# Performance work log

Hardware: AMD Instinct MI355X
Metric: run time of the kernel (lower is better)

Reference implementation:

```python
import jax, jax.numpy as jnp
import numpy as np

B, L, NC = 65536, 1024, 4
C_PHYS = 4000.0       # wave speed in PhysicsConsistencyLoss
WIN = 20              # window_size
SAMPLE_RATE = 20000
C_WE, DX, DT = 1.0, 0.1, 0.01  # WaveEquationLoss defaults
W_WAVE, W_PHYS = 0.1, 0.1


def setup_inputs() -> dict:
    key = jax.random.key(0)
    k1, k2, k3, k4 = jax.random.split(key, 4)
    waveform = jax.random.normal(k1, (B, L), dtype=jnp.float32)
    logits = jax.random.normal(k2, (B, NC), dtype=jnp.float32)
    # depths in [0, 100) -> t_positions = depth*10 in [0, 1000), inside the 1024-sample trace
    defect_depth = jax.random.uniform(k3, (B, 1), dtype=jnp.float32) * 100.0
    labels = jax.random.randint(k4, (B,), 0, NC, dtype=jnp.int64)
    return {"waveform": waveform, "logits": logits,
            "defect_depth": defect_depth, "labels": labels}


def _second_diff(w):
    # interior: w[i+1] - 2 w[i] + w[i-1]; boundaries replicate the torch code exactly
    inner = w[:, 2:] - 2.0 * w[:, 1:-1] + w[:, :-2]
    b0 = (w[:, 1] - w[:, 0])[:, None]          # w1 - 2w0 + w0
    bL = (w[:, -2] - w[:, -1])[:, None]        # w[-1] - 2w[-1] + w[-2]
    return jnp.concatenate([b0, inner, bL], axis=1)


def _wave_eq_loss(w):
    d2 = _second_diff(w)
    d2u_dt2 = d2 / (DT ** 2)
    d2u_dx2 = d2 / (DX ** 2)
    residual = d2u_dt2 - (C_WE ** 2) * d2u_dx2
    return jnp.mean(residual ** 2)


def _physics_consistency_loss(waveform, pred_depth, pred_class):
    bsz, length = waveform.shape
    t_positions = (2.0 * pred_depth[:, 0] / C_PHYS) * SAMPLE_RATE   # (B,)
    t = jnp.linspace(0.0, length - 1, length, dtype=waveform.dtype)  # (L,)
    sigma = WIN / 4.0
    win = jnp.exp(-0.5 * ((t[None, :] - t_positions[:, None]) / sigma) ** 2)  # (B, L)
    win = win / jnp.sum(win, axis=1, keepdims=True)
    energies = jnp.sum(waveform ** 2 * win, axis=1)          # (B,)
    energies = energies / (WIN * jnp.max(waveform))
    is_defect = (pred_class == 2) | (pred_class == 3)
    pen_defect = jnp.where(energies < 0.1, (0.1 - energies) ** 2, 0.0)
    pen_clean = jnp.where(energies > 0.5, (energies - 0.5) ** 2, 0.0)
    penalty = jnp.where(is_defect, pen_defect, pen_clean)
    return jnp.sum(penalty) / bsz


def reference(waveform, logits, defect_depth, labels):
    # masked cross-entropy (labels == -1 ignored)
    mask = labels != -1
    safe_labels = jnp.where(mask, labels, 0)
    logp = jax.nn.log_softmax(logits, axis=-1)
    nll = -jnp.take_along_axis(logp, safe_labels[:, None], axis=1)[:, 0]
    n_valid = jnp.sum(mask)
    cls_loss = jnp.where(n_valid > 0,
                         jnp.sum(jnp.where(mask, nll, 0.0)) / jnp.maximum(n_valid, 1),
                         0.0)
    wave_loss = _wave_eq_loss(waveform)
    pred_class = jnp.argmax(logits, axis=1)
    physics_loss = _physics_consistency_loss(waveform, defect_depth, pred_class)
    total = cls_loss + W_WAVE * wave_loss + W_PHYS * physics_loss
    return (total, cls_loss, wave_loss, physics_loss)
```

## Files before the change

### kernel.cpp

```cpp
#include <hip/hip_runtime.h>
#include <math.h>

#define NROWS 65536
#define LLEN  1024
#define RBLOCKS (NROWS / 8)
#define CBLOCKS (NROWS / 256)

struct Acc {
    double d2_sum;
    float  gmax;
};

__device__ __forceinline__ void row_compute(const float4* f, int lane, float tpos,
                                            float& d2s, float& mx,
                                            float& wsum, float& wesum) {
    d2s = 0.0f; mx = -INFINITY; wsum = 0.0f; wesum = 0.0f;
#pragma unroll
    for (int p = 0; p < 4; ++p) {
        const float x0 = f[p].x, x1 = f[p].y, x2 = f[p].z, x3 = f[p].w;

        float left  = __shfl_up(x3, 1, 64);
        float right = __shfl_down(x0, 1, 64);
        const float prevTail = __shfl((p > 0) ? f[p - 1].w : x0, 63, 64);
        const float nextHead = __shfl((p < 3) ? f[p + 1].x : x3, 0, 64);
        if (lane == 0)  left  = (p > 0) ? prevTail : x0;
        if (lane == 63) right = (p < 3) ? nextHead : x2;

        const float d2a = x1 - 2.0f * x0 + left;
        const float d2b = x2 - 2.0f * x1 + x0;
        const float d2c = x3 - 2.0f * x2 + x1;
        const float d2d = right - 2.0f * x3 + x2;
        d2s += d2a * d2a + d2b * d2b + d2c * d2c + d2d * d2d;

        mx = fmaxf(fmaxf(mx, fmaxf(x0, x1)), fmaxf(x2, x3));

        const float pstart = (float)(p * 256);
        if (tpos > pstart - 75.0f && tpos < pstart + 330.0f) {
            const float e0 = pstart + (float)(4 * lane);
#pragma unroll
            for (int j = 0; j < 4; ++j) {
                const float c = (j == 0) ? x0 : (j == 1) ? x1 : (j == 2) ? x2 : x3;
                const float dt = (e0 + (float)j - tpos) * 0.2f;
                const float g = __expf(-0.5f * dt * dt);
                wsum  += g;
                wesum += c * c * g;
            }
        }
    }
}

__global__ __launch_bounds__(256) void row_kernel(const float* __restrict__ wf,
                                                  const float* __restrict__ depth,
                                                  float* __restrict__ eraw,
                                                  float* __restrict__ d2_part,
                                                  float* __restrict__ mx_part) {
    __shared__ float s_d2[4], s_mx[4];
    const int wave = threadIdx.x >> 6;
    const int lane = threadIdx.x & 63;
    const int r0 = (blockIdx.x * 4 + wave) * 2;

    const float4* srcA = (const float4*)(wf + (size_t)r0 * LLEN);
    const float4* srcB = srcA + (LLEN / 4);
    float4 fA[4], fB[4];
#pragma unroll
    for (int p = 0; p < 4; ++p) fA[p] = srcA[p * 64 + lane];
#pragma unroll
    for (int p = 0; p < 4; ++p) fB[p] = srcB[p * 64 + lane];
    const float2 dep = *(const float2*)(depth + r0);

    float d2sA, mxA, wsA, weA, d2sB, mxB, wsB, weB;
    row_compute(fA, lane, dep.x * 10.0f, d2sA, mxA, wsA, weA);
    row_compute(fB, lane, dep.y * 10.0f, d2sB, mxB, wsB, weB);

#pragma unroll
    for (int off = 32; off > 0; off >>= 1) {
        wsA += __shfl_down(wsA, off, 64);
        weA += __shfl_down(weA, off, 64);
        wsB += __shfl_down(wsB, off, 64);
        weB += __shfl_down(weB, off, 64);
    }
    float d2s = d2sA + d2sB;
    float mx  = fmaxf(mxA, mxB);
#pragma unroll
    for (int off = 32; off > 0; off >>= 1) {
        d2s += __shfl_down(d2s, off, 64);
        mx = fmaxf(mx, __shfl_down(mx, off, 64));
    }

    if (lane == 0) {
        eraw[r0]     = weA / wsA;
        eraw[r0 + 1] = weB / wsB;
        s_d2[wave] = d2s;
        s_mx[wave] = mx;
    }
    __syncthreads();
    if (threadIdx.x == 0) {
        d2_part[blockIdx.x] = s_d2[0] + s_d2[1] + s_d2[2] + s_d2[3];
        mx_part[blockIdx.x] = fmaxf(fmaxf(s_mx[0], s_mx[1]), fmaxf(s_mx[2], s_mx[3]));
    }
}

__global__ __launch_bounds__(256) void reduce_kernel(const float* __restrict__ d2_part,
                                                     const float* __restrict__ mx_part,
                                                     Acc* __restrict__ acc) {
    __shared__ double s_d2[4];
    __shared__ float  s_mx[4];
    const int wave = threadIdx.x >> 6;
    const int lane = threadIdx.x & 63;

    double d2 = 0.0;
    float mx = -INFINITY;
    for (int i = threadIdx.x; i < RBLOCKS; i += 256) {
        d2 += (double)d2_part[i];
        mx = fmaxf(mx, mx_part[i]);
    }
#pragma unroll
    for (int off = 32; off > 0; off >>= 1) {
        d2 += __shfl_down(d2, off, 64);
        mx = fmaxf(mx, __shfl_down(mx, off, 64));
    }
    if (lane == 0) { s_d2[wave] = d2; s_mx[wave] = mx; }
    __syncthreads();
    if (threadIdx.x == 0) {
        acc->d2_sum = s_d2[0] + s_d2[1] + s_d2[2] + s_d2[3];
        acc->gmax   = fmaxf(fmaxf(s_mx[0], s_mx[1]), fmaxf(s_mx[2], s_mx[3]));
    }
}

__global__ __launch_bounds__(256) void cls_kernel(const float* __restrict__ logits,
                                                  const int* __restrict__ labels,
                                                  const float* __restrict__ eraw,
                                                  const Acc* __restrict__ acc,
                                                  float* __restrict__ nll_part,
                                                  float* __restrict__ pen_part,
                                                  int* __restrict__ nv_part) {
    __shared__ float s_nll[4], s_pen[4];
    __shared__ int   s_nv[4];
    const int wave = threadIdx.x >> 6;
    const int lane = threadIdx.x & 63;
    const int r = blockIdx.x * 256 + threadIdx.x;

    const float4 lg = ((const float4*)logits)[r];
    const float m = fmaxf(fmaxf(lg.x, lg.y), fmaxf(lg.z, lg.w));
    const float lse = m + logf(__expf(lg.x - m) + __expf(lg.y - m) +
                               __expf(lg.z - m) + __expf(lg.w - m));

    const int lab = labels[r];
    const bool valid = (lab != -1);
    const int sl = valid ? lab : 0;
    const float lv = (sl == 0) ? lg.x : (sl == 1) ? lg.y : (sl == 2) ? lg.z : lg.w;
    float nll = valid ? (lse - lv) : 0.0f;

    int pc = 0; float bv = lg.x;
    if (lg.y > bv) { bv = lg.y; pc = 1; }
    if (lg.z > bv) { bv = lg.z; pc = 2; }
    if (lg.w > bv) { bv = lg.w; pc = 3; }

    const float E = eraw[r] / (20.0f * acc->gmax);
    const bool isdef = (pc == 2) || (pc == 3);
    float pen;
    if (isdef) pen = (E < 0.1f) ? (0.1f - E) * (0.1f - E) : 0.0f;
    else       pen = (E > 0.5f) ? (E - 0.5f) * (E - 0.5f) : 0.0f;

    const unsigned long long bal = __ballot(valid);
#pragma unroll
    for (int off = 32; off > 0; off >>= 1) {
        nll += __shfl_down(nll, off, 64);
        pen += __shfl_down(pen, off, 64);
    }
    if (lane == 0) { s_nll[wave] = nll; s_pen[wave] = pen; s_nv[wave] = __popcll(bal); }
    __syncthreads();
    if (threadIdx.x == 0) {
        nll_part[blockIdx.x] = s_nll[0] + s_nll[1] + s_nll[2] + s_nll[3];
        pen_part[blockIdx.x] = s_pen[0] + s_pen[1] + s_pen[2] + s_pen[3];
        nv_part[blockIdx.x]  = s_nv[0] + s_nv[1] + s_nv[2] + s_nv[3];
    }
}

__global__ __launch_bounds__(256) void final_kernel(const float* __restrict__ nll_part,
                                                    const float* __restrict__ pen_part,
                                                    const int* __restrict__ nv_part,
                                                    const Acc* __restrict__ acc,
                                                    float* __restrict__ out) {
    __shared__ double s_nll[4], s_pen[4];
    __shared__ int    s_nv[4];
    const int wave = threadIdx.x >> 6;
    const int lane = threadIdx.x & 63;

    double nll = (double)nll_part[threadIdx.x];
    double pen = (double)pen_part[threadIdx.x];
    int nv = nv_part[threadIdx.x];
#pragma unroll
    for (int off = 32; off > 0; off >>= 1) {
        nll += __shfl_down(nll, off, 64);
        pen += __shfl_down(pen, off, 64);
        nv  += __shfl_down(nv,  off, 64);
    }
    if (lane == 0) { s_nll[wave] = nll; s_pen[wave] = pen; s_nv[wave] = nv; }
    __syncthreads();
    if (threadIdx.x == 0) {
        const double nll_s = s_nll[0] + s_nll[1] + s_nll[2] + s_nll[3];
        const double pen_s = s_pen[0] + s_pen[1] + s_pen[2] + s_pen[3];
        const int    nv_s  = s_nv[0] + s_nv[1] + s_nv[2] + s_nv[3];
        const double cls  = (nv_s > 0) ? nll_s / (double)nv_s : 0.0;
        const double wave_l = acc->d2_sum * (9900.0 * 9900.0) / ((double)NROWS * (double)LLEN);
        const double phys = pen_s / (double)NROWS;
        out[0] = (float)(cls + 0.1 * wave_l + 0.1 * phys);
        out[1] = (float)cls;
        out[2] = (float)wave_l;
        out[3] = (float)phys;
    }
}

extern "C" void kernel_launch(void* const* d_in, const int* in_sizes, int n_in,
                              void* d_out, int out_size, void* d_ws, size_t ws_size,
                              hipStream_t stream) {
    const float* wf     = (const float*)d_in[0];
    const float* logits = (const float*)d_in[1];
    const float* depth  = (const float*)d_in[2];
    const int*   labels = (const int*)d_in[3];
    float* out = (float*)d_out;

    char* ws = (char*)d_ws;
    Acc*   acc      = (Acc*)ws;                       ws += 256;
    float* eraw     = (float*)ws;                     ws += NROWS * sizeof(float);
    float* d2_part  = (float*)ws;                     ws += RBLOCKS * sizeof(float);
    float* mx_part  = (float*)ws;                     ws += RBLOCKS * sizeof(float);
    float* nll_part = (float*)ws;                     ws += CBLOCKS * sizeof(float);
    float* pen_part = (float*)ws;                     ws += CBLOCKS * sizeof(float);
    int*   nv_part  = (int*)ws;

    row_kernel<<<RBLOCKS, 256, 0, stream>>>(wf, depth, eraw, d2_part, mx_part);
    reduce_kernel<<<1, 256, 0, stream>>>(d2_part, mx_part, acc);
    cls_kernel<<<CBLOCKS, 256, 0, stream>>>(logits, labels, eraw, acc, nll_part, pen_part, nv_part);
    final_kernel<<<1, 256, 0, stream>>>(nll_part, pen_part, nv_part, acc, out);
}
```

Baseline: 371.9 us.

## Fuse classification into row kernel and collapse reductions into one last-block fold kernel

Moves the cross-entropy and argmax work into the row kernel, computed by two lanes per wave, and packs the defect flag into the sign bit of the stored energy. The separate reduce, classification and final kernels are replaced by one fold kernel. That kernel does a two-level partial reduction, and the last block, found through an atomic counter, computes the penalty over all rows serially. This cuts two kernel launches and the extra logits pass. The cost is a single block walking all 65536 energies at the end, plus reliance on a counter that is reset inside row_kernel.

```diff
diff --git a/kernel.cpp b/kernel.cpp
--- a/kernel.cpp
+++ b/kernel.cpp
@@ -4,12 +4,7 @@
 #define NROWS 65536
 #define LLEN  1024
 #define RBLOCKS (NROWS / 8)
-#define CBLOCKS (NROWS / 256)
-
-struct Acc {
-    double d2_sum;
-    float  gmax;
-};
+#define FBLOCKS 256
 
 __device__ __forceinline__ void row_compute(const float4* f, int lane, float tpos,
                                             float& d2s, float& mx,
@@ -50,15 +45,22 @@
 }
 
 __global__ __launch_bounds__(256) void row_kernel(const float* __restrict__ wf,
+                                                  const float* __restrict__ logits,
                                                   const float* __restrict__ depth,
+                                                  const int* __restrict__ labels,
                                                   float* __restrict__ eraw,
                                                   float* __restrict__ d2_part,
-                                                  float* __restrict__ mx_part) {
-    __shared__ float s_d2[4], s_mx[4];
+                                                  float* __restrict__ mx_part,
+                                                  float* __restrict__ nll_part,
+                                                  float* __restrict__ nv_part,
+                                                  unsigned int* __restrict__ counter) {
+    __shared__ float s_d2[4], s_mx[4], s_nll[4], s_nv[4];
     const int wave = threadIdx.x >> 6;
     const int lane = threadIdx.x & 63;
     const int r0 = (blockIdx.x * 4 + wave) * 2;
 
+    if (blockIdx.x == 0 && threadIdx.x == 0) *counter = 0u;
+
     const float4* srcA = (const float4*)(wf + (size_t)r0 * LLEN);
     const float4* srcB = srcA + (LLEN / 4);
     float4 fA[4], fB[4];
@@ -67,6 +69,27 @@
 #pragma unroll
     for (int p = 0; p < 4; ++p) fB[p] = srcB[p * 64 + lane];
     const float2 dep = *(const float2*)(depth + r0);
+
+    float nll = 0.0f, nv = 0.0f;
+    bool isdef = false;
+    if (lane < 2) {
+        const int r = r0 + lane;
+        const float4 lg = ((const float4*)logits)[r];
+        const float m = fmaxf(fmaxf(lg.x, lg.y), fmaxf(lg.z, lg.w));
+        const float lse = m + logf(__expf(lg.x - m) + __expf(lg.y - m) +
+                                   __expf(lg.z - m) + __expf(lg.w - m));
+        const int lab = labels[r];
+        const bool valid = (lab != -1);
+        const int sl = valid ? lab : 0;
+        const float lv = (sl == 0) ? lg.x : (sl == 1) ? lg.y : (sl == 2) ? lg.z : lg.w;
+        nll = valid ? (lse - lv) : 0.0f;
+        nv  = valid ? 1.0f : 0.0f;
+        int pc = 0; float bv = lg.x;
+        if (lg.y > bv) { bv = lg.y; pc = 1; }
+        if (lg.z > bv) { bv = lg.z; pc = 2; }
+        if (lg.w > bv) { bv = lg.w; pc = 3; }
+        isdef = (pc == 2) || (pc == 3);
+    }
 
     float d2sA, mxA, wsA, weA, d2sB, mxB, wsB, weB;
     row_compute(fA, lane, dep.x * 10.0f, d2sA, mxA, wsA, weA);
@@ -86,125 +109,126 @@
         d2s += __shfl_down(d2s, off, 64);
         mx = fmaxf(mx, __shfl_down(mx, off, 64));
     }
-
+    const float wsB0 = __shfl(wsB, 0, 64);
+    const float weB0 = __shfl(weB, 0, 64);
+    const float nll01 = nll + __shfl_down(nll, 1, 64);
+    const float nv01  = nv  + __shfl_down(nv, 1, 64);
+
+    if (lane < 2) {
+        const float e = (lane == 0) ? (weA / wsA) : (weB0 / wsB0);
+        const unsigned int bits = __float_as_uint(e) | (isdef ? 0x80000000u : 0u);
+        eraw[r0 + lane] = __uint_as_float(bits);
+    }
     if (lane == 0) {
-        eraw[r0]     = weA / wsA;
-        eraw[r0 + 1] = weB / wsB;
-        s_d2[wave] = d2s;
-        s_mx[wave] = mx;
+        s_d2[wave] = d2s;  s_mx[wave] = mx;
+        s_nll[wave] = nll01;  s_nv[wave] = nv01;
     }
     __syncthreads();
     if (threadIdx.x == 0) {
-        d2_part[blockIdx.x] = s_d2[0] + s_d2[1] + s_d2[2] + s_d2[3];
-        mx_part[blockIdx.x] = fmaxf(fmaxf(s_mx[0], s_mx[1]), fmaxf(s_mx[2], s_mx[3]));
-    }
-}
-
-__global__ __launch_bounds__(256) void reduce_kernel(const float* __restrict__ d2_part,
-                                                     const float* __restrict__ mx_part,
-                                                     Acc* __restrict__ acc) {
-    __shared__ double s_d2[4];
-    __shared__ float  s_mx[4];
+        d2_part[blockIdx.x]  = s_d2[0] + s_d2[1] + s_d2[2] + s_d2[3];
+        mx_part[blockIdx.x]  = fmaxf(fmaxf(s_mx[0], s_mx[1]), fmaxf(s_mx[2], s_mx[3]));
+        nll_part[blockIdx.x] = s_nll[0] + s_nll[1] + s_nll[2] + s_nll[3];
+        nv_part[blockIdx.x]  = s_nv[0] + s_nv[1] + s_nv[2] + s_nv[3];
+    }
+}
+
+__global__ __launch_bounds__(256) void fold_kernel(const float* __restrict__ d2_part,
+                                                   const float* __restrict__ mx_part,
+                                                   const float* __restrict__ nll_part,
+                                                   const float* __restrict__ nv_part,
+                                                   const float* __restrict__ eraw,
+                                                   double* __restrict__ d2_p2,
+                                                   float* __restrict__ mx_p2,
+                                                   double* __restrict__ nll_p2,
+                                                   float* __restrict__ nv_p2,
+                                                   unsigned int* __restrict__ counter,
+                                                   float* __restrict__ out) {
     const int wave = threadIdx.x >> 6;
     const int lane = threadIdx.x & 63;
 
-    double d2 = 0.0;
-    float mx = -INFINITY;
-    for (int i = threadIdx.x; i < RBLOCKS; i += 256) {
-        d2 += (double)d2_part[i];
-        mx = fmaxf(mx, mx_part[i]);
-    }
-#pragma unroll
-    for (int off = 32; off > 0; off >>= 1) {
-        d2 += __shfl_down(d2, off, 64);
-        mx = fmaxf(mx, __shfl_down(mx, off, 64));
-    }
-    if (lane == 0) { s_d2[wave] = d2; s_mx[wave] = mx; }
+    {
+        const int base = blockIdx.x * 32;
+        double d2 = 0.0, nl = 0.0;
+        float mx = -INFINITY, nv = 0.0f;
+        if (threadIdx.x < 32) {
+            const int i = base + threadIdx.x;
+            d2 = (double)d2_part[i];
+            nl = (double)nll_part[i];
+            mx = mx_part[i];
+            nv = nv_part[i];
+        }
+        if (wave == 0) {
+#pragma unroll
+            for (int off = 16; off > 0; off >>= 1) {
+                d2 += __shfl_down(d2, off, 64);
+                nl += __shfl_down(nl, off, 64);
+                nv += __shfl_down(nv, off, 64);
+                mx = fmaxf(mx, __shfl_down(mx, off, 64));
+            }
+            if (lane == 0) {
+                d2_p2[blockIdx.x] = d2;
+                nll_p2[blockIdx.x] = nl;
+                mx_p2[blockIdx.x] = mx;
+                nv_p2[blockIdx.x] = nv;
+            }
+        }
+    }
+    __threadfence();
+    __shared__ bool amLast;
+    if (threadIdx.x == 0)
+        amLast = (atomicAdd(counter, 1u) == FBLOCKS - 1);
+    __syncthreads();
+    if (!amLast) return;
+    __threadfence();
+
+    __shared__ double sh_d2[4], sh_nll[4];
+    __shared__ float sh_mx[4], sh_nv[4];
+    __shared__ float sh_gmax;
+    __shared__ double sh_base[3];
+    {
+        double d2 = d2_p2[threadIdx.x];
+        double nl = nll_p2[threadIdx.x];
+        float mx = mx_p2[threadIdx.x];
+        float nv = nv_p2[threadIdx.x];
+#pragma unroll
+        for (int off = 32; off > 0; off >>= 1) {
+            d2 += __shfl_down(d2, off, 64);
+            nl += __shfl_down(nl, off, 64);
+            nv += __shfl_down(nv, off, 64);
+            mx = fmaxf(mx, __shfl_down(mx, off, 64));
+        }
+        if (lane == 0) { sh_d2[wave] = d2; sh_nll[wave] = nl; sh_mx[wave] = mx; sh_nv[wave] = nv; }
+    }
     __syncthreads();
     if (threadIdx.x == 0) {
-        acc->d2_sum = s_d2[0] + s_d2[1] + s_d2[2] + s_d2[3];
-        acc->gmax   = fmaxf(fmaxf(s_mx[0], s_mx[1]), fmaxf(s_mx[2], s_mx[3]));
-    }
-}
-
-__global__ __launch_bounds__(256) void cls_kernel(const float* __restrict__ logits,
-                                                  const int* __restrict__ labels,
-                                                  const float* __restrict__ eraw,
-                                                  const Acc* __restrict__ acc,
-                                                  float* __restrict__ nll_part,
-                                                  float* __restrict__ pen_part,
-                                                  int* __restrict__ nv_part) {
-    __shared__ float s_nll[4], s_pen[4];
-    __shared__ int   s_nv[4];
-    const int wave = threadIdx.x >> 6;
-    const int lane = threadIdx.x & 63;
-    const int r = blockIdx.x * 256 + threadIdx.x;
-
-    const float4 lg = ((const float4*)logits)[r];
-    const float m = fmaxf(fmaxf(lg.x, lg.y), fmaxf(lg.z, lg.w));
-    const float lse = m + logf(__expf(lg.x - m) + __expf(lg.y - m) +
-                               __expf(lg.z - m) + __expf(lg.w - m));
-
-    const int lab = labels[r];
-    const bool valid = (lab != -1);
-    const int sl = valid ? lab : 0;
-    const float lv = (sl == 0) ? lg.x : (sl == 1) ? lg.y : (sl == 2) ? lg.z : lg.w;
-    float nll = valid ? (lse - lv) : 0.0f;
-
-    int pc = 0; float bv = lg.x;
-    if (lg.y > bv) { bv = lg.y; pc = 1; }
-    if (lg.z > bv) { bv = lg.z; pc = 2; }
-    if (lg.w > bv) { bv = lg.w; pc = 3; }
-
-    const float E = eraw[r] / (20.0f * acc->gmax);
-    const bool isdef = (pc == 2) || (pc == 3);
-    float pen;
-    if (isdef) pen = (E < 0.1f) ? (0.1f - E) * (0.1f - E) : 0.0f;
-    else       pen = (E > 0.5f) ? (E - 0.5f) * (E - 0.5f) : 0.0f;
-
-    const unsigned long long bal = __ballot(valid);
-#pragma unroll
-    for (int off = 32; off > 0; off >>= 1) {
-        nll += __shfl_down(nll, off, 64);
-        pen += __shfl_down(pen, off, 64);
-    }
-    if (lane == 0) { s_nll[wave] = nll; s_pen[wave] = pen; s_nv[wave] = __popcll(bal); }
+        const double d2_sum = sh_d2[0] + sh_d2[1] + sh_d2[2] + sh_d2[3];
+        const double nll_sum = sh_nll[0] + sh_nll[1] + sh_nll[2] + sh_nll[3];
+        const float nv_sum = sh_nv[0] + sh_nv[1] + sh_nv[2] + sh_nv[3];
+        sh_gmax = fmaxf(fmaxf(sh_mx[0], sh_mx[1]), fmaxf(sh_mx[2], sh_mx[3]));
+        sh_base[0] = (nv_sum > 0.0f) ? nll_sum / (double)nv_sum : 0.0;
+        sh_base[1] = d2_sum * (9900.0 * 9900.0) / ((double)NROWS * (double)LLEN);
+    }
+    __syncthreads();
+    const float inv20g = 1.0f / (20.0f * sh_gmax);
+
+    float pen = 0.0f;
+    for (int r = threadIdx.x; r < NROWS; r += 256) {
+        const float v = eraw[r];
+        const bool isdef = signbit(v);
+        const float E = fabsf(v) * inv20g;
+        if (isdef) pen += (E < 0.1f) ? (0.1f - E) * (0.1f - E) : 0.0f;
+        else       pen += (E > 0.5f) ? (E - 0.5f) * (E - 0.5f) : 0.0f;
+    }
+    __shared__ double sh_pen[4];
+    double pend = (double)pen;
+#pragma unroll
+    for (int off = 32; off > 0; off >>= 1) pend += __shfl_down(pend, off, 64);
+    if (lane == 0) sh_pen[wave] = pend;
     __syncthreads();
     if (threadIdx.x == 0) {
-        nll_part[blockIdx.x] = s_nll[0] + s_nll[1] + s_nll[2] + s_nll[3];
-        pen_part[blockIdx.x] = s_pen[0] + s_pen[1] + s_pen[2] + s_pen[3];
-        nv_part[blockIdx.x]  = s_nv[0] + s_nv[1] + s_nv[2] + s_nv[3];
-    }
-}
-
-__global__ __launch_bounds__(256) void final_kernel(const float* __restrict__ nll_part,
-                                                    const float* __restrict__ pen_part,
-                                                    const int* __restrict__ nv_part,
-                                                    const Acc* __restrict__ acc,
-                                                    float* __restrict__ out) {
-    __shared__ double s_nll[4], s_pen[4];
-    __shared__ int    s_nv[4];
-    const int wave = threadIdx.x >> 6;
-    const int lane = threadIdx.x & 63;
-
-    double nll = (double)nll_part[threadIdx.x];
-    double pen = (double)pen_part[threadIdx.x];
-    int nv = nv_part[threadIdx.x];
-#pragma unroll
-    for (int off = 32; off > 0; off >>= 1) {
-        nll += __shfl_down(nll, off, 64);
-        pen += __shfl_down(pen, off, 64);
-        nv  += __shfl_down(nv,  off, 64);
-    }
-    if (lane == 0) { s_nll[wave] = nll; s_pen[wave] = pen; s_nv[wave] = nv; }
-    __syncthreads();
-    if (threadIdx.x == 0) {
-        const double nll_s = s_nll[0] + s_nll[1] + s_nll[2] + s_nll[3];
-        const double pen_s = s_pen[0] + s_pen[1] + s_pen[2] + s_pen[3];
-        const int    nv_s  = s_nv[0] + s_nv[1] + s_nv[2] + s_nv[3];
-        const double cls  = (nv_s > 0) ? nll_s / (double)nv_s : 0.0;
-        const double wave_l = acc->d2_sum * (9900.0 * 9900.0) / ((double)NROWS * (double)LLEN);
-        const double phys = pen_s / (double)NROWS;
+        const double phys = (sh_pen[0] + sh_pen[1] + sh_pen[2] + sh_pen[3]) / (double)NROWS;
+        const double cls = sh_base[0];
+        const double wave_l = sh_base[1];
         out[0] = (float)(cls + 0.1 * wave_l + 0.1 * phys);
         out[1] = (float)cls;
         out[2] = (float)wave_l;
@@ -222,16 +246,19 @@
     float* out = (float*)d_out;
 
     char* ws = (char*)d_ws;
-    Acc*   acc      = (Acc*)ws;                       ws += 256;
+    unsigned int* counter = (unsigned int*)ws;        ws += 256;
     float* eraw     = (float*)ws;                     ws += NROWS * sizeof(float);
     float* d2_part  = (float*)ws;                     ws += RBLOCKS * sizeof(float);
     float* mx_part  = (float*)ws;                     ws += RBLOCKS * sizeof(float);
-    float* nll_part = (float*)ws;                     ws += CBLOCKS * sizeof(float);
-    float* pen_part = (float*)ws;                     ws += CBLOCKS * sizeof(float);
-    int*   nv_part  = (int*)ws;
-
-    row_kernel<<<RBLOCKS, 256, 0, stream>>>(wf, depth, eraw, d2_part, mx_part);
-    reduce_kernel<<<1, 256, 0, stream>>>(d2_part, mx_part, acc);
-    cls_kernel<<<CBLOCKS, 256, 0, stream>>>(logits, labels, eraw, acc, nll_part, pen_part, nv_part);
-    final_kernel<<<1, 256, 0, stream>>>(nll_part, pen_part, nv_part, acc, out);
-}
+    float* nll_part = (float*)ws;                     ws += RBLOCKS * sizeof(float);
+    float* nv_part  = (float*)ws;                     ws += RBLOCKS * sizeof(float);
+    double* d2_p2   = (double*)ws;                    ws += FBLOCKS * sizeof(double);
+    double* nll_p2  = (double*)ws;                    ws += FBLOCKS * sizeof(double);
+    float* mx_p2    = (float*)ws;                     ws += FBLOCKS * sizeof(float);
+    float* nv_p2    = (float*)ws;
+
+    row_kernel<<<RBLOCKS, 256, 0, stream>>>(wf, logits, depth, labels, eraw,
+                                            d2_part, mx_part, nll_part, nv_part, counter);
+    fold_kernel<<<FBLOCKS, 256, 0, stream>>>(d2_part, mx_part, nll_part, nv_part, eraw,
+                                             d2_p2, mx_p2, nll_p2, nv_p2, counter, out);
+}
```

After: 458.9 us. 23.4% more time.
